# Kernel optimization log

Measured on AMD Instinct MI355X. Metric: run time of the kernel, lower is better.

Reference implementation:

```python
import jax, jax.numpy as jnp
import numpy as np


def setup_inputs() -> dict:
    key = jax.random.key(0)
    ks = jax.random.split(key, 9)
    B, L, D, H, E = 8, 2048, 1024, 256, 8
    Hg = D // 4
    s = 0.02
    return {
        "x": jax.random.normal(ks[0], (B, L, D), dtype=jnp.float32),
        "wg1": jax.random.normal(ks[1], (D, Hg), dtype=jnp.float32) * s,
        "bg1": jax.random.normal(ks[2], (Hg,), dtype=jnp.float32) * s,
        "wg2": jax.random.normal(ks[3], (Hg, E), dtype=jnp.float32) * s,
        "bg2": jax.random.normal(ks[4], (E,), dtype=jnp.float32) * s,
        "w1": jax.random.normal(ks[5], (E, D, H), dtype=jnp.float32) * (1.0 / np.sqrt(D)),
        "b1": jax.random.normal(ks[6], (E, H), dtype=jnp.float32) * s,
        "w2": jax.random.normal(ks[7], (E, H, D), dtype=jnp.float32) * (1.0 / np.sqrt(H)),
        "b2": jax.random.normal(ks[8], (E, D), dtype=jnp.float32) * s,
        "k": 2,
    }


def reference(x, wg1, bg1, wg2, bg2, w1, b1, w2, b2, k):
    B, L, D = x.shape
    xt = x.reshape(-1, D)                       # [T, D] tokens
    T = xt.shape[0]
    # gating MLP: Linear -> GELU(exact, matches torch nn.GELU) -> Linear -> softmax
    logits = jax.nn.gelu(xt @ wg1 + bg1, approximate=False) @ wg2 + bg2  # [T, E]
    scores = jax.nn.softmax(logits, axis=-1)
    top_v, top_i = jax.lax.top_k(scores, k)     # [T, k]
    # dense gate matrix (equivalent to compute_gating's scatter); zeros for non-top-k
    gates = jnp.zeros_like(scores).at[jnp.arange(T)[:, None], top_i].set(top_v)  # [T, E]

    # grouped-GEMM MoE: y[t] = sum_e gates[t,e] * (gelu(x[t] @ W1_e + b1_e) @ W2_e + b2_e)
    # scan over the fixed, small expert axis; gates zero out non-selected experts,
    # giving math identical to the sort/dispatch + per-expert torch.mm loop.
    def body(acc, we):
        w1e, b1e, w2e, b2e, ge = we
        h = jax.nn.gelu(xt @ w1e + b1e, approximate=False)  # [T, H]
        o = h @ w2e + b2e                                    # [T, D]
        return acc + ge[:, None] * o, None

    y, _ = jax.lax.scan(body, jnp.zeros_like(xt), (w1, b1, w2, b2, gates.T))
    return y.reshape(B, L, D)
```

## Files before the change

kernel.cpp:

```cpp
#include <hip/hip_runtime.h>

typedef unsigned short u16;
typedef __attribute__((ext_vector_type(8))) short bf16x8;
typedef __attribute__((ext_vector_type(4))) float f32x4;
typedef __attribute__((ext_vector_type(4))) u16 u16x4;

#define T_TOK 16384
#define D_DIM 1024
#define NE 8
#define MAXP 33792

__device__ __forceinline__ u16 f2bf(float f) {
  union { float f; unsigned int u; } c; c.f = f;
  unsigned int u = c.u;
  u += 0x7fffu + ((u >> 16) & 1u);
  return (u16)(u >> 16);
}

__device__ __forceinline__ float bf2f(u16 v) {
  union { unsigned int u; float f; } c; c.u = ((unsigned int)v) << 16;
  return c.f;
}

__device__ __forceinline__ float gelu_exact(float u) {
  return 0.5f * u * (1.0f + erff(u * 0.70710678118654752f));
}

__device__ __forceinline__ void gld16(const void* g, void* l) {
  __builtin_amdgcn_global_load_lds(
      (const __attribute__((address_space(1))) unsigned int*)g,
      (__attribute__((address_space(3))) unsigned int*)l, 16, 0, 0);
}


__device__ __forceinline__ void stage_tile_swz(u16* lds, const char* g0, size_t stride,
                                               int wid, int lane) {
  const int rg = lane >> 3;
  const int cs = ((lane & 7) ^ rg) * 16;
  const char* g = g0 + (size_t)(wid * 8 + rg) * stride + cs;
  char* l = (char*)lds + wid * 1024;
  #pragma unroll
  for (int c = 0; c < 4; ++c)
    gld16(g + (size_t)(32 * c) * stride, l + c * 4096);
}

__device__ __forceinline__ bf16x8 rd_swz(const u16* lds, int row, int colu16) {
  const int byte = (row * 128 + colu16 * 2) ^ ((row & 7) << 4);
  return *(const bf16x8*)((const char*)lds + byte);
}

__device__ __forceinline__ void mma_step_swz(const u16* As, const u16* Bs, f32x4 acc[4][4],
                                             int wm, int wn, int lane) {
  const int r = lane & 15, kq = (lane >> 4) * 8;
  #pragma unroll
  for (int ks = 0; ks < 2; ++ks) {
    const int col = ks * 32 + kq;
    bf16x8 a[4], b[4];
    #pragma unroll
    for (int mf = 0; mf < 4; ++mf)
      a[mf] = rd_swz(As, wm * 64 + mf * 16 + r, col);
    #pragma unroll
    for (int nf = 0; nf < 4; ++nf)
      b[nf] = rd_swz(Bs, wn * 64 + nf * 16 + r, col);
    #pragma unroll
    for (int mf = 0; mf < 4; ++mf)
      #pragma unroll
      for (int nf = 0; nf < 4; ++nf)
        acc[mf][nf] = __builtin_amdgcn_mfma_f32_16x16x32_bf16(a[mf], b[nf], acc[mf][nf], 0, 0, 0);
  }
}

__device__ __forceinline__ void mma_64x128_swz(const u16* As, const u16* Bs, f32x4 acc[2][4],
                                               int wm, int wn, int lane) {
  const int r = lane & 15, kq = (lane >> 4) * 8;
  #pragma unroll
  for (int ks = 0; ks < 2; ++ks) {
    const int col = ks * 32 + kq;
    bf16x8 a[2], b[4];
    #pragma unroll
    for (int mf = 0; mf < 2; ++mf)
      a[mf] = rd_swz(As, wm * 32 + mf * 16 + r, col);
    #pragma unroll
    for (int nf = 0; nf < 4; ++nf)
      b[nf] = rd_swz(Bs, wn * 64 + nf * 16 + r, col);
    #pragma unroll
    for (int mf = 0; mf < 2; ++mf)
      #pragma unroll
      for (int nf = 0; nf < 4; ++nf)
        acc[mf][nf] = __builtin_amdgcn_mfma_f32_16x16x32_bf16(a[mf], b[nf], acc[mf][nf], 0, 0, 0);
  }
}

__device__ __forceinline__ void stage_b64x32(u16* lds, const u16* mat, int rowbase,
                                             int k0, int wid, int lane) {
  const int row = wid * 16 + (lane >> 2);
  const char* g = (const char*)(mat + (size_t)(rowbase + row) * 1024 + k0 + (lane & 3) * 8);
  char* l = (char*)lds + wid * 1024;
  gld16(g, l);
}

__device__ __forceinline__ void stage_b32(u16* lds, const u16* mat, int rowbase,
                                          int k0, int wid, int lane) {
  const char* g0 = (const char*)(mat + (size_t)rowbase * 1024 + k0);
  #pragma unroll
  for (int c = 0; c < 2; ++c) {
    const int row = c * 64 + wid * 16 + (lane >> 2);
    const char* g = g0 + (size_t)row * 2048 + (size_t)((lane & 3) * 16);
    char* l = (char*)lds + c * 4096 + wid * 1024;
    gld16(g, l);
  }
}

__global__ __launch_bounds__(256) void cvt_hilo_x_kernel(const float* __restrict__ x,
                                                         u16* __restrict__ xh,
                                                         u16* __restrict__ xl) {
  const int i = (blockIdx.x * 256 + threadIdx.x) * 4;
  float4 v = *(const float4*)(x + i);
  float vv[4] = {v.x, v.y, v.z, v.w};
  u16x4 h, l;
  u16 hh[4], ll[4];
  #pragma unroll
  for (int q = 0; q < 4; ++q) { hh[q] = f2bf(vv[q]); ll[q] = f2bf(vv[q] - bf2f(hh[q])); }
  h.x = hh[0]; h.y = hh[1]; h.z = hh[2]; h.w = hh[3];
  l.x = ll[0]; l.y = ll[1]; l.z = ll[2]; l.w = ll[3];
  *(u16x4*)(xh + i) = h;
  *(u16x4*)(xl + i) = l;
}

__global__ __launch_bounds__(256) void transpose_cvt_kernel(const float* __restrict__ in,
                                                            u16* __restrict__ out,
                                                            int R, int C) {
  __shared__ u16 t[32][36];
  const int e = blockIdx.z;
  const int r0 = blockIdx.x * 32, c0 = blockIdx.y * 32;
  const int tid = threadIdx.x;
  {
    const int r = tid >> 3, cq = (tid & 7) * 4;
    float4 v = *(const float4*)(in + ((size_t)e * R + r0 + r) * C + c0 + cq);
    t[r][cq + 0] = f2bf(v.x); t[r][cq + 1] = f2bf(v.y);
    t[r][cq + 2] = f2bf(v.z); t[r][cq + 3] = f2bf(v.w);
  }
  __syncthreads();
  {
    const int c = tid >> 3, rq = (tid & 7) * 4;
    u16x4 o;
    o.x = t[rq + 0][c]; o.y = t[rq + 1][c]; o.z = t[rq + 2][c]; o.w = t[rq + 3][c];
    *(u16x4*)(out + ((size_t)e * C + c0 + c) * R + r0 + rq) = o;
  }
}

__global__ __launch_bounds__(256) void transpose_hilo_kernel(const float* __restrict__ in,
                                                             u16* __restrict__ out_hi,
                                                             u16* __restrict__ out_lo,
                                                             int R, int C) {
  __shared__ u16 th[32][36];
  __shared__ u16 tl[32][36];
  const int r0 = blockIdx.x * 32, c0 = blockIdx.y * 32;
  const int tid = threadIdx.x;
  {
    const int r = tid >> 3, cq = (tid & 7) * 4;
    float4 v = *(const float4*)(in + (size_t)(r0 + r) * C + c0 + cq);
    float vv[4] = {v.x, v.y, v.z, v.w};
    #pragma unroll
    for (int i = 0; i < 4; ++i) {
      u16 h = f2bf(vv[i]);
      th[r][cq + i] = h;
      tl[r][cq + i] = f2bf(vv[i] - bf2f(h));
    }
  }
  __syncthreads();
  {
    const int c = tid >> 3, rq = (tid & 7) * 4;
    u16x4 oh, ol;
    oh.x = th[rq + 0][c]; oh.y = th[rq + 1][c]; oh.z = th[rq + 2][c]; oh.w = th[rq + 3][c];
    ol.x = tl[rq + 0][c]; ol.y = tl[rq + 1][c]; ol.z = tl[rq + 2][c]; ol.w = tl[rq + 3][c];
    *(u16x4*)(out_hi + (size_t)(c0 + c) * R + r0 + rq) = oh;
    *(u16x4*)(out_lo + (size_t)(c0 + c) * R + r0 + rq) = ol;
  }
}

__global__ __launch_bounds__(256) void gating_mfma_kernel(
    const u16* __restrict__ xh, const u16* __restrict__ xl,
    const u16* __restrict__ wg1t_hi, const u16* __restrict__ wg1t_lo,
    float* __restrict__ p_buf) {
  __shared__ u16 Ah[64 * 32], Al[64 * 32];
  __shared__ u16 Bh[128 * 32], Bl[128 * 32];
  const int tid = threadIdx.x, lane = tid & 63, wid = tid >> 6;
  const int t0 = blockIdx.x * 64, n0 = blockIdx.y * 128;
  const int kh = blockIdx.z, kbeg = kh * 512;
  const int wm = wid >> 1, wn = wid & 1;

  f32x4 acc[2][4];
  #pragma unroll
  for (int i = 0; i < 2; ++i)
    #pragma unroll
    for (int j = 0; j < 4; ++j) acc[i][j] = (f32x4){0.f, 0.f, 0.f, 0.f};

  for (int kt = 0; kt < 16; ++kt) {
    const int k0 = kbeg + kt * 32;
    __syncthreads();
    stage_b64x32(Ah, xh, t0, k0, wid, lane);
    stage_b64x32(Al, xl, t0, k0, wid, lane);
    stage_b32(Bh, wg1t_hi, n0, k0, wid, lane);
    stage_b32(Bl, wg1t_lo, n0, k0, wid, lane);
    __syncthreads();
    const int r = lane & 15, ko = (lane >> 4) * 8;
    bf16x8 ah[2], al[2];
    #pragma unroll
    for (int mf = 0; mf < 2; ++mf) {
      const int ro = (wm * 32 + mf * 16 + r) * 32 + ko;
      ah[mf] = *(const bf16x8*)&Ah[ro];
      al[mf] = *(const bf16x8*)&Al[ro];
    }
    #pragma unroll
    for (int nf = 0; nf < 4; ++nf) {
      const int ro = (wn * 64 + nf * 16 + r) * 32 + ko;
      bf16x8 bh = *(const bf16x8*)&Bh[ro];
      bf16x8 bl = *(const bf16x8*)&Bl[ro];
      #pragma unroll
      for (int mf = 0; mf < 2; ++mf) {
        acc[mf][nf] = __builtin_amdgcn_mfma_f32_16x16x32_bf16(ah[mf], bh, acc[mf][nf], 0, 0, 0);
        acc[mf][nf] = __builtin_amdgcn_mfma_f32_16x16x32_bf16(ah[mf], bl, acc[mf][nf], 0, 0, 0);
        acc[mf][nf] = __builtin_amdgcn_mfma_f32_16x16x32_bf16(al[mf], bh, acc[mf][nf], 0, 0, 0);
      }
    }
  }

  #pragma unroll
  for (int mf = 0; mf < 2; ++mf)
    #pragma unroll
    for (int rr = 0; rr < 4; ++rr) {
      const int lt = wm * 32 + mf * 16 + ((lane >> 4) << 2) + rr;
      #pragma unroll
      for (int nf = 0; nf < 4; ++nf) {
        const int ln = wn * 64 + nf * 16 + (lane & 15);
        p_buf[((size_t)kh * T_TOK + t0 + lt) * 256 + n0 + ln] = acc[mf][nf][rr];
      }
    }
}

__global__ __launch_bounds__(256) void gating_p2_kernel(
    const float* __restrict__ p_buf, const float* __restrict__ bg1,
    const float* __restrict__ wg2, const float* __restrict__ bg2,
    int* __restrict__ top_i, float2* __restrict__ top_g) {
  const int tid = threadIdx.x;
  const int tn = tid & 31, tm = tid >> 5;
  const int t0 = blockIdx.x * 32;

  float bb[8];
  {
    float4 ba = *(const float4*)&bg1[tn * 4];
    float4 bc = *(const float4*)&bg1[128 + tn * 4];
    bb[0] = ba.x; bb[1] = ba.y; bb[2] = ba.z; bb[3] = ba.w;
    bb[4] = bc.x; bb[5] = bc.y; bb[6] = bc.z; bb[7] = bc.w;
  }

  float hv[4][8];
  #pragma unroll
  for (int i = 0; i < 4; ++i) {
    const size_t t = t0 + tm * 4 + i;
    const float* pa = &p_buf[t * 256];
    const float* pb = &p_buf[((size_t)T_TOK + t) * 256];
    float4 a0 = *(const float4*)&pa[tn * 4];
    float4 a1 = *(const float4*)&pa[128 + tn * 4];
    float4 b0 = *(const float4*)&pb[tn * 4];
    float4 b1 = *(const float4*)&pb[128 + tn * 4];
    hv[i][0] = gelu_exact(a0.x + b0.x + bb[0]);
    hv[i][1] = gelu_exact(a0.y + b0.y + bb[1]);
    hv[i][2] = gelu_exact(a0.z + b0.z + bb[2]);
    hv[i][3] = gelu_exact(a0.w + b0.w + bb[3]);
    hv[i][4] = gelu_exact(a1.x + b1.x + bb[4]);
    hv[i][5] = gelu_exact(a1.y + b1.y + bb[5]);
    hv[i][6] = gelu_exact(a1.z + b1.z + bb[6]);
    hv[i][7] = gelu_exact(a1.w + b1.w + bb[7]);
  }

  float part[4][8];
  #pragma unroll
  for (int i = 0; i < 4; ++i)
    #pragma unroll
    for (int e = 0; e < 8; ++e) part[i][e] = 0.f;
  #pragma unroll
  for (int j = 0; j < 8; ++j) {
    const int col = (j < 4) ? (tn * 4 + j) : (128 + tn * 4 + (j - 4));
    float4 wa = *(const float4*)&wg2[col * 8];
    float4 wb = *(const float4*)&wg2[col * 8 + 4];
    float we[8] = {wa.x, wa.y, wa.z, wa.w, wb.x, wb.y, wb.z, wb.w};
    #pragma unroll
    for (int i = 0; i < 4; ++i)
      #pragma unroll
      for (int e = 0; e < 8; ++e) part[i][e] += hv[i][j] * we[e];
  }
  #pragma unroll
  for (int mask = 1; mask < 32; mask <<= 1)
    #pragma unroll
    for (int i = 0; i < 4; ++i)
      #pragma unroll
      for (int e = 0; e < 8; ++e) part[i][e] += __shfl_xor(part[i][e], mask);

  if (tn < 4) {
    float lg[8];
    #pragma unroll
    for (int i = 0; i < 4; ++i)
      if (tn == i) {
        #pragma unroll
        for (int e = 0; e < 8; ++e) lg[e] = part[i][e];
      }
    #pragma unroll
    for (int e = 0; e < 8; ++e) lg[e] += bg2[e];
    float m = lg[0];
    #pragma unroll
    for (int e = 1; e < 8; ++e) m = fmaxf(m, lg[e]);
    float ex[8], s = 0.f;
    #pragma unroll
    for (int e = 0; e < 8; ++e) { ex[e] = expf(lg[e] - m); s += ex[e]; }
    int i1 = 0;
    #pragma unroll
    for (int e = 1; e < 8; ++e) if (lg[e] > lg[i1]) i1 = e;
    int i2 = (i1 == 0) ? 1 : 0;
    #pragma unroll
    for (int e = 0; e < 8; ++e) if (e != i1 && lg[e] > lg[i2]) i2 = e;
    float inv = 1.f / s;
    const int t = t0 + tm * 4 + tn;
    top_i[t] = i1 | (i2 << 8);
    top_g[t] = make_float2(ex[i1] * inv, ex[i2] * inv);
  }
}

__global__ __launch_bounds__(256) void hist_kernel(const int* __restrict__ top_i,
                                                   int* __restrict__ hist) {
  __shared__ int h[NE];
  const int tid = threadIdx.x;
  if (tid < NE) h[tid] = 0;
  __syncthreads();
  const int ti = top_i[blockIdx.x * 256 + tid];
  atomicAdd(&h[ti & 255], 1);
  atomicAdd(&h[ti >> 8], 1);
  __syncthreads();
  if (tid < NE) hist[blockIdx.x * NE + tid] = h[tid];
}

__global__ __launch_bounds__(64) void scan_kernel(const int* __restrict__ hist,
                                                  int* __restrict__ cnt,
                                                  int* __restrict__ offs,
                                                  int* __restrict__ cbase) {
  __shared__ int tot[NE], off_s[NE];
  const int tid = threadIdx.x;
  if (tid < NE) {
    int s = 0;
    for (int c = 0; c < 64; ++c) s += hist[c * NE + tid];
    tot[tid] = s; cnt[tid] = s;
  }
  __syncthreads();
  if (tid == 0) {
    int o = 0;
    #pragma unroll
    for (int e = 0; e < NE; ++e) { off_s[e] = o; o += (tot[e] + 127) & ~127; }
  }
  __syncthreads();
  if (tid < NE) {
    offs[tid] = off_s[tid];
    int r = off_s[tid];
    for (int c = 0; c < 64; ++c) { cbase[c * NE + tid] = r; r += hist[c * NE + tid]; }
  }
}

__global__ __launch_bounds__(256) void fill_kernel(
    const int* __restrict__ top_i, const int* __restrict__ cbase,
    int* __restrict__ tok_list, int* __restrict__ pos1, int* __restrict__ pos2) {
  __shared__ int lcnt[NE];
  const int tid = threadIdx.x;
  if (tid < NE) lcnt[tid] = 0;
  __syncthreads();
  const int t = blockIdx.x * 256 + tid;
  const int ti = top_i[t];
  const int i1 = ti & 255, i2 = ti >> 8;
  const int r1 = atomicAdd(&lcnt[i1], 1);
  const int r2 = atomicAdd(&lcnt[i2], 1);
  const int p1 = cbase[blockIdx.x * NE + i1] + r1;
  const int p2 = cbase[blockIdx.x * NE + i2] + r2;
  tok_list[p1] = t; tok_list[p2] = t;
  pos1[t] = p1; pos2[t] = p2;
}

__global__ __launch_bounds__(256) void expert_h_kernel(
    const u16* __restrict__ xb, const u16* __restrict__ w1t,
    const float* __restrict__ b1, const int* __restrict__ tok_list,
    const int* __restrict__ cnt, const int* __restrict__ offs,
    u16* __restrict__ h_c) {
  __shared__ u16 As[64 * 64];
  __shared__ u16 Bs[128 * 64];
  __shared__ float b1_s[128];
  const int e = blockIdx.z;
  const int nblk = (cnt[e] + 63) >> 6;
  if ((int)blockIdx.x >= nblk) return;
  const int tid = threadIdx.x, lane = tid & 63, wid = tid >> 6;
  const int base = offs[e] + blockIdx.x * 64;
  const int n0 = blockIdx.y * 128;
  const int wm = wid >> 1, wn = wid & 1;

  if (tid < 128) b1_s[tid] = b1[e * 256 + n0 + tid];

  int tk[2];
  #pragma unroll
  for (int c = 0; c < 2; ++c)
    tk[c] = tok_list[base + (wid * 2 + c) * 8 + (lane >> 3)];

  f32x4 acc[2][4];
  #pragma unroll
  for (int i = 0; i < 2; ++i)
    #pragma unroll
    for (int j = 0; j < 4; ++j) acc[i][j] = (f32x4){0.f, 0.f, 0.f, 0.f};

  const char* Bb = (const char*)w1t + ((size_t)e * 256 + n0) * 2048;
  const int cb = ((lane & 7) ^ ((lane >> 3) & 7)) * 16;
  for (int kt = 0; kt < 16; ++kt) {
    __syncthreads();
    {
      char* l = (char*)As + wid * 2048;
      #pragma unroll
      for (int c = 0; c < 2; ++c)
        gld16((const char*)xb + (size_t)tk[c] * 2048 + kt * 128 + cb, l + c * 1024);
    }
    stage_tile_swz(Bs, Bb + kt * 128, 2048, wid, lane);
    __syncthreads();
    mma_64x128_swz(As, Bs, acc, wm, wn, lane);
  }

  #pragma unroll
  for (int mf = 0; mf < 2; ++mf)
    #pragma unroll
    for (int rr = 0; rr < 4; ++rr) {
      const int lt = wm * 32 + mf * 16 + ((lane >> 4) << 2) + rr;
      #pragma unroll
      for (int nf = 0; nf < 4; ++nf) {
        const int ln = wn * 64 + nf * 16 + (lane & 15);
        float u = acc[mf][nf][rr] + b1_s[ln];
        h_c[(size_t)(base + lt) * 256 + n0 + ln] = f2bf(gelu_exact(u));
      }
    }
}

__global__ __launch_bounds__(256) void moe_out_kernel(
    const u16* __restrict__ h_c, const u16* __restrict__ w2t,
    const float* __restrict__ b2, const int* __restrict__ cnt,
    const int* __restrict__ offs, u16* __restrict__ o_c) {
  __shared__ u16 As[128 * 64];
  __shared__ u16 Bs[128 * 64];
  __shared__ float b2_s[128];
  const int e = blockIdx.z;
  const int nblk = (cnt[e] + 127) >> 7;
  if ((int)blockIdx.x >= nblk) return;
  const int tid = threadIdx.x, lane = tid & 63, wid = tid >> 6;
  const int base = offs[e] + blockIdx.x * 128;
  const int n0 = blockIdx.y * 128;
  const int wm = wid >> 1, wn = wid & 1;

  if (tid < 128) b2_s[tid] = b2[(size_t)e * 1024 + n0 + tid];

  f32x4 acc[4][4];
  #pragma unroll
  for (int i = 0; i < 4; ++i)
    #pragma unroll
    for (int j = 0; j < 4; ++j) acc[i][j] = (f32x4){0.f, 0.f, 0.f, 0.f};

  const char* Ab = (const char*)h_c + (size_t)base * 512;
  const char* Bb = (const char*)w2t + ((size_t)e * D_DIM + n0) * 512;
  #pragma unroll 1
  for (int kt = 0; kt < 4; ++kt) {
    __syncthreads();
    stage_tile_swz(As, Ab + kt * 128, 512, wid, lane);
    stage_tile_swz(Bs, Bb + kt * 128, 512, wid, lane);
    __syncthreads();
    mma_step_swz(As, Bs, acc, wm, wn, lane);
  }

  #pragma unroll
  for (int mf = 0; mf < 4; ++mf)
    #pragma unroll
    for (int rr = 0; rr < 4; ++rr) {
      const int lt = wm * 64 + mf * 16 + ((lane >> 4) << 2) + rr;
      #pragma unroll
      for (int nf = 0; nf < 4; ++nf) {
        const int ln = wn * 64 + nf * 16 + (lane & 15);
        o_c[(size_t)(base + lt) * 1024 + n0 + ln] = f2bf(acc[mf][nf][rr] + b2_s[ln]);
      }
    }
}

__global__ __launch_bounds__(256) void gather_kernel(
    const u16* __restrict__ o_c, const int* __restrict__ pos1,
    const int* __restrict__ pos2, const float2* __restrict__ top_g,
    float* __restrict__ y) {
  const int t = blockIdx.x;
  const int p1 = pos1[t], p2 = pos2[t];
  const float2 g = top_g[t];
  const int c = threadIdx.x * 4;
  u16x4 a = *(const u16x4*)&o_c[(size_t)p1 * 1024 + c];
  u16x4 b = *(const u16x4*)&o_c[(size_t)p2 * 1024 + c];
  float4 o;
  o.x = g.x * bf2f(a.x) + g.y * bf2f(b.x);
  o.y = g.x * bf2f(a.y) + g.y * bf2f(b.y);
  o.z = g.x * bf2f(a.z) + g.y * bf2f(b.z);
  o.w = g.x * bf2f(a.w) + g.y * bf2f(b.w);
  *(float4*)&y[(size_t)t * 1024 + c] = o;
}

extern "C" void kernel_launch(void* const* d_in, const int* in_sizes, int n_in,
                              void* d_out, int out_size, void* d_ws, size_t ws_size,
                              hipStream_t stream) {
  (void)in_sizes; (void)n_in; (void)out_size; (void)ws_size;
  const float* x   = (const float*)d_in[0];
  const float* wg1 = (const float*)d_in[1];
  const float* bg1 = (const float*)d_in[2];
  const float* wg2 = (const float*)d_in[3];
  const float* bg2 = (const float*)d_in[4];
  const float* w1  = (const float*)d_in[5];
  const float* b1  = (const float*)d_in[6];
  const float* w2  = (const float*)d_in[7];
  const float* b2  = (const float*)d_in[8];
  float* y = (float*)d_out;

  char* ws = (char*)d_ws;
  u16* xb   = (u16*)(ws);
  u16* w1t  = (u16*)(ws + 33554432);
  u16* w2t  = (u16*)(ws + 37748736);
  char* M   = ws + 41943040;
  int*    cnt      = (int*)(M);
  int*    offs     = (int*)(M + 64);
  int*    hist     = (int*)(M + 128);
  int*    cbase    = (int*)(M + 2304);
  int*    tok_list = (int*)(M + 4608);
  int*    top_i    = (int*)(M + 139776);
  float2* top_g    = (float2*)(M + 205312);
  int*    pos1     = (int*)(M + 336384);
  int*    pos2     = (int*)(M + 401920);
  u16* h_c = (u16*)(ws + 42467328);
  u16* o_c = (u16*)(ws + 59768832);
  float* p_buf   = (float*)(ws + 59768832);
  u16*   wg1t_hi = (u16*)(ws + 93323264);
  u16*   wg1t_lo = (u16*)(ws + 93847552);
  u16*   xl      = (u16*)(ws + 94371840);

  hipMemsetAsync(tok_list, 0, 135168, stream);
  cvt_hilo_x_kernel<<<16384, 256, 0, stream>>>(x, xb, xl);
  transpose_cvt_kernel<<<dim3(32, 8, 8), 256, 0, stream>>>(w1, w1t, 1024, 256);
  transpose_cvt_kernel<<<dim3(8, 32, 8), 256, 0, stream>>>(w2, w2t, 256, 1024);
  transpose_hilo_kernel<<<dim3(32, 8), 256, 0, stream>>>(wg1, wg1t_hi, wg1t_lo, 1024, 256);
  gating_mfma_kernel<<<dim3(256, 2, 2), 256, 0, stream>>>(xb, xl, wg1t_hi, wg1t_lo, p_buf);
  gating_p2_kernel<<<512, 256, 0, stream>>>(p_buf, bg1, wg2, bg2, top_i, top_g);
  hist_kernel<<<64, 256, 0, stream>>>(top_i, hist);
  scan_kernel<<<1, 64, 0, stream>>>(hist, cnt, offs, cbase);
  fill_kernel<<<64, 256, 0, stream>>>(top_i, cbase, tok_list, pos1, pos2);
  expert_h_kernel<<<dim3(256, 2, 8), 256, 0, stream>>>(xb, w1t, b1, tok_list, cnt, offs, h_c);
  moe_out_kernel <<<dim3(128, 8, 8), 256, 0, stream>>>(h_c, w2t, b2, cnt, offs, o_c);
  gather_kernel  <<<16384, 256, 0, stream>>>(o_c, pos1, pos2, top_g, y);
}
```

Measured before the change: 195.1 us.

## Fuse expert up-projection and down-projection into one kernel with hidden in LDS

```diff
diff --git a/kernel.cpp b/kernel.cpp
--- a/kernel.cpp
+++ b/kernel.cpp
@@ -49,46 +49,13 @@
   return *(const bf16x8*)((const char*)lds + byte);
 }
 
-__device__ __forceinline__ void mma_step_swz(const u16* As, const u16* Bs, f32x4 acc[4][4],
-                                             int wm, int wn, int lane) {
-  const int r = lane & 15, kq = (lane >> 4) * 8;
-  #pragma unroll
-  for (int ks = 0; ks < 2; ++ks) {
-    const int col = ks * 32 + kq;
-    bf16x8 a[4], b[4];
-    #pragma unroll
-    for (int mf = 0; mf < 4; ++mf)
-      a[mf] = rd_swz(As, wm * 64 + mf * 16 + r, col);
-    #pragma unroll
-    for (int nf = 0; nf < 4; ++nf)
-      b[nf] = rd_swz(Bs, wn * 64 + nf * 16 + r, col);
-    #pragma unroll
-    for (int mf = 0; mf < 4; ++mf)
-      #pragma unroll
-      for (int nf = 0; nf < 4; ++nf)
-        acc[mf][nf] = __builtin_amdgcn_mfma_f32_16x16x32_bf16(a[mf], b[nf], acc[mf][nf], 0, 0, 0);
-  }
-}
-
-__device__ __forceinline__ void mma_64x128_swz(const u16* As, const u16* Bs, f32x4 acc[2][4],
-                                               int wm, int wn, int lane) {
-  const int r = lane & 15, kq = (lane >> 4) * 8;
-  #pragma unroll
-  for (int ks = 0; ks < 2; ++ks) {
-    const int col = ks * 32 + kq;
-    bf16x8 a[2], b[4];
-    #pragma unroll
-    for (int mf = 0; mf < 2; ++mf)
-      a[mf] = rd_swz(As, wm * 32 + mf * 16 + r, col);
-    #pragma unroll
-    for (int nf = 0; nf < 4; ++nf)
-      b[nf] = rd_swz(Bs, wn * 64 + nf * 16 + r, col);
-    #pragma unroll
-    for (int mf = 0; mf < 2; ++mf)
-      #pragma unroll
-      for (int nf = 0; nf < 4; ++nf)
-        acc[mf][nf] = __builtin_amdgcn_mfma_f32_16x16x32_bf16(a[mf], b[nf], acc[mf][nf], 0, 0, 0);
-  }
+__device__ __forceinline__ bf16x8 rd_swz512(const u16* lds, int row, int colu16) {
+  const int byte = (row * 512 + colu16 * 2) ^ ((row & 7) << 4);
+  return *(const bf16x8*)((const char*)lds + byte);
+}
+__device__ __forceinline__ void wr_swz512(u16* lds, int row, int colu16, u16 v) {
+  const int byte = (row * 512 + colu16 * 2) ^ ((row & 7) << 4);
+  *(u16*)((char*)lds + byte) = v;
 }
 
 __device__ __forceinline__ void stage_b64x32(u16* lds, const u16* mat, int rowbase,
@@ -109,6 +76,13 @@
     char* l = (char*)lds + c * 4096 + wid * 1024;
     gld16(g, l);
   }
+}
+
+__device__ __forceinline__ int find_expert(const int* offs, int p0) {
+  int e = 0;
+  #pragma unroll
+  for (int q = 1; q < NE; ++q) if (p0 >= offs[q]) e = q;
+  return e;
 }
 
 __global__ __launch_bounds__(256) void cvt_hilo_x_kernel(const float* __restrict__ x,
@@ -383,109 +357,128 @@
   pos1[t] = p1; pos2[t] = p2;
 }
 
-__global__ __launch_bounds__(256) void expert_h_kernel(
+__global__ __launch_bounds__(256) void fused_expert_kernel(
     const u16* __restrict__ xb, const u16* __restrict__ w1t,
-    const float* __restrict__ b1, const int* __restrict__ tok_list,
+    const u16* __restrict__ w2t, const float* __restrict__ b1,
+    const float* __restrict__ b2, const int* __restrict__ tok_list,
     const int* __restrict__ cnt, const int* __restrict__ offs,
-    u16* __restrict__ h_c) {
-  __shared__ u16 As[64 * 64];
-  __shared__ u16 Bs[128 * 64];
-  __shared__ float b1_s[128];
-  const int e = blockIdx.z;
-  const int nblk = (cnt[e] + 63) >> 6;
-  if ((int)blockIdx.x >= nblk) return;
+    u16* __restrict__ o_c) {
+  __shared__ u16 AB[20480];
+  __shared__ u16 h_lds[64 * 256];
+  __shared__ float b1_s[256];
+  u16* As = AB;
+  u16* Bs = AB + 4096;
+  u16* B2s = AB;
+
   const int tid = threadIdx.x, lane = tid & 63, wid = tid >> 6;
-  const int base = offs[e] + blockIdx.x * 64;
-  const int n0 = blockIdx.y * 128;
+  const int base = blockIdx.x * 64;
+  const int e = find_expert(offs, base);
+  if (base >= offs[e] + ((cnt[e] + 127) & ~127)) return;
   const int wm = wid >> 1, wn = wid & 1;
-
-  if (tid < 128) b1_s[tid] = b1[e * 256 + n0 + tid];
+  const int r = lane & 15, kq = (lane >> 4) * 8;
+
+  b1_s[tid] = b1[e * 256 + tid];
 
   int tk[2];
   #pragma unroll
   for (int c = 0; c < 2; ++c)
     tk[c] = tok_list[base + (wid * 2 + c) * 8 + (lane >> 3)];
-
-  f32x4 acc[2][4];
-  #pragma unroll
-  for (int i = 0; i < 2; ++i)
-    #pragma unroll
-    for (int j = 0; j < 4; ++j) acc[i][j] = (f32x4){0.f, 0.f, 0.f, 0.f};
-
-  const char* Bb = (const char*)w1t + ((size_t)e * 256 + n0) * 2048;
   const int cb = ((lane & 7) ^ ((lane >> 3) & 7)) * 16;
-  for (int kt = 0; kt < 16; ++kt) {
-    __syncthreads();
-    {
-      char* l = (char*)As + wid * 2048;
-      #pragma unroll
-      for (int c = 0; c < 2; ++c)
-        gld16((const char*)xb + (size_t)tk[c] * 2048 + kt * 128 + cb, l + c * 1024);
-    }
-    stage_tile_swz(Bs, Bb + kt * 128, 2048, wid, lane);
-    __syncthreads();
-    mma_64x128_swz(As, Bs, acc, wm, wn, lane);
-  }
-
-  #pragma unroll
-  for (int mf = 0; mf < 2; ++mf)
-    #pragma unroll
-    for (int rr = 0; rr < 4; ++rr) {
-      const int lt = wm * 32 + mf * 16 + ((lane >> 4) << 2) + rr;
-      #pragma unroll
-      for (int nf = 0; nf < 4; ++nf) {
-        const int ln = wn * 64 + nf * 16 + (lane & 15);
-        float u = acc[mf][nf][rr] + b1_s[ln];
-        h_c[(size_t)(base + lt) * 256 + n0 + ln] = f2bf(gelu_exact(u));
-      }
-    }
-}
-
-__global__ __launch_bounds__(256) void moe_out_kernel(
-    const u16* __restrict__ h_c, const u16* __restrict__ w2t,
-    const float* __restrict__ b2, const int* __restrict__ cnt,
-    const int* __restrict__ offs, u16* __restrict__ o_c) {
-  __shared__ u16 As[128 * 64];
-  __shared__ u16 Bs[128 * 64];
-  __shared__ float b2_s[128];
-  const int e = blockIdx.z;
-  const int nblk = (cnt[e] + 127) >> 7;
-  if ((int)blockIdx.x >= nblk) return;
-  const int tid = threadIdx.x, lane = tid & 63, wid = tid >> 6;
-  const int base = offs[e] + blockIdx.x * 128;
-  const int n0 = blockIdx.y * 128;
-  const int wm = wid >> 1, wn = wid & 1;
-
-  if (tid < 128) b2_s[tid] = b2[(size_t)e * 1024 + n0 + tid];
-
-  f32x4 acc[4][4];
-  #pragma unroll
-  for (int i = 0; i < 4; ++i)
-    #pragma unroll
-    for (int j = 0; j < 4; ++j) acc[i][j] = (f32x4){0.f, 0.f, 0.f, 0.f};
-
-  const char* Ab = (const char*)h_c + (size_t)base * 512;
-  const char* Bb = (const char*)w2t + ((size_t)e * D_DIM + n0) * 512;
-  #pragma unroll 1
-  for (int kt = 0; kt < 4; ++kt) {
-    __syncthreads();
-    stage_tile_swz(As, Ab + kt * 128, 512, wid, lane);
-    stage_tile_swz(Bs, Bb + kt * 128, 512, wid, lane);
-    __syncthreads();
-    mma_step_swz(As, Bs, acc, wm, wn, lane);
-  }
-
-  #pragma unroll
-  for (int mf = 0; mf < 4; ++mf)
-    #pragma unroll
-    for (int rr = 0; rr < 4; ++rr) {
-      const int lt = wm * 64 + mf * 16 + ((lane >> 4) << 2) + rr;
-      #pragma unroll
-      for (int nf = 0; nf < 4; ++nf) {
-        const int ln = wn * 64 + nf * 16 + (lane & 15);
-        o_c[(size_t)(base + lt) * 1024 + n0 + ln] = f2bf(acc[mf][nf][rr] + b2_s[ln]);
-      }
-    }
+
+  {
+    f32x4 acc1[2][8];
+    #pragma unroll
+    for (int i = 0; i < 2; ++i)
+      #pragma unroll
+      for (int j = 0; j < 8; ++j) acc1[i][j] = (f32x4){0.f, 0.f, 0.f, 0.f};
+
+    const char* Bb = (const char*)w1t + (size_t)e * 256 * 2048;
+    for (int kt = 0; kt < 16; ++kt) {
+      __syncthreads();
+      {
+        char* l = (char*)As + wid * 2048;
+        #pragma unroll
+        for (int c = 0; c < 2; ++c)
+          gld16((const char*)xb + (size_t)tk[c] * 2048 + kt * 128 + cb, l + c * 1024);
+      }
+      stage_tile_swz(Bs, Bb + kt * 128, 2048, wid, lane);
+      stage_tile_swz(Bs + 128 * 64, Bb + 128 * 2048 + kt * 128, 2048, wid, lane);
+      __syncthreads();
+      #pragma unroll
+      for (int ks = 0; ks < 2; ++ks) {
+        const int col = ks * 32 + kq;
+        bf16x8 a[2], b[8];
+        #pragma unroll
+        for (int mf = 0; mf < 2; ++mf)
+          a[mf] = rd_swz(As, wm * 32 + mf * 16 + r, col);
+        #pragma unroll
+        for (int nf = 0; nf < 8; ++nf)
+          b[nf] = rd_swz(Bs, wn * 128 + nf * 16 + r, col);
+        #pragma unroll
+        for (int mf = 0; mf < 2; ++mf)
+          #pragma unroll
+          for (int nf = 0; nf < 8; ++nf)
+            acc1[mf][nf] = __builtin_amdgcn_mfma_f32_16x16x32_bf16(a[mf], b[nf], acc1[mf][nf], 0, 0, 0);
+      }
+    }
+    #pragma unroll
+    for (int mf = 0; mf < 2; ++mf)
+      #pragma unroll
+      for (int rr = 0; rr < 4; ++rr) {
+        const int row = wm * 32 + mf * 16 + ((lane >> 4) << 2) + rr;
+        #pragma unroll
+        for (int nf = 0; nf < 8; ++nf) {
+          const int colc = wn * 128 + nf * 16 + (lane & 15);
+          float u = acc1[mf][nf][rr] + b1_s[colc];
+          wr_swz512(h_lds, row, colc, f2bf(gelu_exact(u)));
+        }
+      }
+  }
+
+  const char* Wb = (const char*)w2t + (size_t)e * D_DIM * 512;
+  for (int nt = 0; nt < 8; ++nt) {
+    const int n0 = nt * 128;
+    f32x4 acc2[2][4];
+    #pragma unroll
+    for (int i = 0; i < 2; ++i)
+      #pragma unroll
+      for (int j = 0; j < 4; ++j) acc2[i][j] = (f32x4){0.f, 0.f, 0.f, 0.f};
+
+    #pragma unroll 1
+    for (int kt = 0; kt < 4; ++kt) {
+      __syncthreads();
+      stage_tile_swz(B2s, Wb + (size_t)n0 * 512 + kt * 128, 512, wid, lane);
+      __syncthreads();
+      #pragma unroll
+      for (int ks = 0; ks < 2; ++ks) {
+        const int col = ks * 32 + kq;
+        bf16x8 a[2], b[4];
+        #pragma unroll
+        for (int mf = 0; mf < 2; ++mf)
+          a[mf] = rd_swz512(h_lds, wm * 32 + mf * 16 + r, kt * 64 + col);
+        #pragma unroll
+        for (int nf = 0; nf < 4; ++nf)
+          b[nf] = rd_swz(B2s, wn * 64 + nf * 16 + r, col);
+        #pragma unroll
+        for (int mf = 0; mf < 2; ++mf)
+          #pragma unroll
+          for (int nf = 0; nf < 4; ++nf)
+            acc2[mf][nf] = __builtin_amdgcn_mfma_f32_16x16x32_bf16(a[mf], b[nf], acc2[mf][nf], 0, 0, 0);
+      }
+    }
+    #pragma unroll
+    for (int nf = 0; nf < 4; ++nf) {
+      const int ln = wn * 64 + nf * 16 + (lane & 15);
+      const float bv = b2[(size_t)e * 1024 + n0 + ln];
+      #pragma unroll
+      for (int mf = 0; mf < 2; ++mf)
+        #pragma unroll
+        for (int rr = 0; rr < 4; ++rr) {
+          const int lt = wm * 32 + mf * 16 + ((lane >> 4) << 2) + rr;
+          o_c[(size_t)(base + lt) * 1024 + n0 + ln] = f2bf(acc2[mf][nf][rr] + bv);
+        }
+    }
+  }
 }
 
 __global__ __launch_bounds__(256) void gather_kernel(
@@ -535,7 +528,6 @@
   float2* top_g    = (float2*)(M + 205312);
   int*    pos1     = (int*)(M + 336384);
   int*    pos2     = (int*)(M + 401920);
-  u16* h_c = (u16*)(ws + 42467328);
   u16* o_c = (u16*)(ws + 59768832);
   float* p_buf   = (float*)(ws + 59768832);
   u16*   wg1t_hi = (u16*)(ws + 93323264);
@@ -552,7 +544,6 @@
   hist_kernel<<<64, 256, 0, stream>>>(top_i, hist);
   scan_kernel<<<1, 64, 0, stream>>>(hist, cnt, offs, cbase);
   fill_kernel<<<64, 256, 0, stream>>>(top_i, cbase, tok_list, pos1, pos2);
-  expert_h_kernel<<<dim3(256, 2, 8), 256, 0, stream>>>(xb, w1t, b1, tok_list, cnt, offs, h_c);
-  moe_out_kernel <<<dim3(128, 8, 8), 256, 0, stream>>>(h_c, w2t, b2, cnt, offs, o_c);
-  gather_kernel  <<<16384, 256, 0, stream>>>(o_c, pos1, pos2, top_g, y);
-}
+  fused_expert_kernel<<<528, 256, 0, stream>>>(xb, w1t, w2t, b1, b2, tok_list, cnt, offs, o_c);
+  gather_kernel<<<16384, 256, 0, stream>>>(o_c, pos1, pos2, top_g, y);
+}
```

Result: slower. 237.2 us (+21.5%).

## Flatten moe_out grid over padded rows and widen tiles to 128x256 with 8 waves

Applied to the files above, without the earlier changes.

```diff
diff --git a/kernel.cpp b/kernel.cpp
--- a/kernel.cpp
+++ b/kernel.cpp
@@ -44,6 +44,27 @@
     gld16(g + (size_t)(32 * c) * stride, l + c * 4096);
 }
 
+__device__ __forceinline__ void stage_a128_8w(u16* lds, const char* g0, size_t stride,
+                                              int wid, int lane) {
+  const int rg = lane >> 3;
+  const int cs = ((lane & 7) ^ rg) * 16;
+  const char* g = g0 + (size_t)(wid * 16 + rg) * stride + cs;
+  char* l = (char*)lds + wid * 2048;
+  gld16(g, l);
+  gld16(g + (size_t)8 * stride, l + 1024);
+}
+
+__device__ __forceinline__ void stage_b256_8w(u16* lds, const char* g0, size_t stride,
+                                              int wid, int lane) {
+  const int rg = lane >> 3;
+  const int cs = ((lane & 7) ^ rg) * 16;
+  const char* g = g0 + (size_t)(wid * 32 + rg) * stride + cs;
+  char* l = (char*)lds + wid * 4096;
+  #pragma unroll
+  for (int c = 0; c < 4; ++c)
+    gld16(g + (size_t)(8 * c) * stride, l + c * 1024);
+}
+
 __device__ __forceinline__ bf16x8 rd_swz(const u16* lds, int row, int colu16) {
   const int byte = (row * 128 + colu16 * 2) ^ ((row & 7) << 4);
   return *(const bf16x8*)((const char*)lds + byte);
@@ -109,6 +130,13 @@
     char* l = (char*)lds + c * 4096 + wid * 1024;
     gld16(g, l);
   }
+}
+
+__device__ __forceinline__ int find_expert(const int* offs, int p0) {
+  int e = 0;
+  #pragma unroll
+  for (int q = 1; q < NE; ++q) if (p0 >= offs[q]) e = q;
+  return e;
 }
 
 __global__ __launch_bounds__(256) void cvt_hilo_x_kernel(const float* __restrict__ x,
@@ -441,22 +469,19 @@
     }
 }
 
-__global__ __launch_bounds__(256) void moe_out_kernel(
+__global__ __launch_bounds__(512) void moe_out_kernel(
     const u16* __restrict__ h_c, const u16* __restrict__ w2t,
     const float* __restrict__ b2, const int* __restrict__ cnt,
     const int* __restrict__ offs, u16* __restrict__ o_c) {
   __shared__ u16 As[128 * 64];
-  __shared__ u16 Bs[128 * 64];
-  __shared__ float b2_s[128];
-  const int e = blockIdx.z;
-  const int nblk = (cnt[e] + 127) >> 7;
-  if ((int)blockIdx.x >= nblk) return;
+  __shared__ u16 Bs[256 * 64];
   const int tid = threadIdx.x, lane = tid & 63, wid = tid >> 6;
-  const int base = offs[e] + blockIdx.x * 128;
-  const int n0 = blockIdx.y * 128;
-  const int wm = wid >> 1, wn = wid & 1;
-
-  if (tid < 128) b2_s[tid] = b2[(size_t)e * 1024 + n0 + tid];
+  const int base = blockIdx.x * 128;
+  const int e = find_expert(offs, base);
+  if (base >= offs[e] + ((cnt[e] + 127) & ~127)) return;
+  const int n0 = blockIdx.y * 256;
+  const int wm = wid >> 2, wn = wid & 3;
+  const int r = lane & 15, kq = (lane >> 4) * 8;
 
   f32x4 acc[4][4];
   #pragma unroll
@@ -469,23 +494,39 @@
   #pragma unroll 1
   for (int kt = 0; kt < 4; ++kt) {
     __syncthreads();
-    stage_tile_swz(As, Ab + kt * 128, 512, wid, lane);
-    stage_tile_swz(Bs, Bb + kt * 128, 512, wid, lane);
+    stage_a128_8w(As, Ab + kt * 128, 512, wid, lane);
+    stage_b256_8w(Bs, Bb + kt * 128, 512, wid, lane);
     __syncthreads();
-    mma_step_swz(As, Bs, acc, wm, wn, lane);
-  }
-
-  #pragma unroll
-  for (int mf = 0; mf < 4; ++mf)
-    #pragma unroll
-    for (int rr = 0; rr < 4; ++rr) {
-      const int lt = wm * 64 + mf * 16 + ((lane >> 4) << 2) + rr;
-      #pragma unroll
-      for (int nf = 0; nf < 4; ++nf) {
-        const int ln = wn * 64 + nf * 16 + (lane & 15);
-        o_c[(size_t)(base + lt) * 1024 + n0 + ln] = f2bf(acc[mf][nf][rr] + b2_s[ln]);
+    #pragma unroll
+    for (int ks = 0; ks < 2; ++ks) {
+      const int col = ks * 32 + kq;
+      bf16x8 a[4], b[4];
+      #pragma unroll
+      for (int mf = 0; mf < 4; ++mf)
+        a[mf] = rd_swz(As, wm * 64 + mf * 16 + r, col);
+      #pragma unroll
+      for (int nf = 0; nf < 4; ++nf)
+        b[nf] = rd_swz(Bs, wn * 64 + nf * 16 + r, col);
+      #pragma unroll
+      for (int mf = 0; mf < 4; ++mf)
+        #pragma unroll
+        for (int nf = 0; nf < 4; ++nf)
+          acc[mf][nf] = __builtin_amdgcn_mfma_f32_16x16x32_bf16(a[mf], b[nf], acc[mf][nf], 0, 0, 0);
+    }
+  }
+
+  #pragma unroll
+  for (int nf = 0; nf < 4; ++nf) {
+    const int ln = wn * 64 + nf * 16 + (lane & 15);
+    const float bv = b2[(size_t)e * 1024 + n0 + ln];
+    #pragma unroll
+    for (int mf = 0; mf < 4; ++mf)
+      #pragma unroll
+      for (int rr = 0; rr < 4; ++rr) {
+        const int lt = wm * 64 + mf * 16 + ((lane >> 4) << 2) + rr;
+        o_c[(size_t)(base + lt) * 1024 + n0 + ln] = f2bf(acc[mf][nf][rr] + bv);
       }
-    }
+  }
 }
 
 __global__ __launch_bounds__(256) void gather_kernel(
@@ -553,6 +594,6 @@
   scan_kernel<<<1, 64, 0, stream>>>(hist, cnt, offs, cbase);
   fill_kernel<<<64, 256, 0, stream>>>(top_i, cbase, tok_list, pos1, pos2);
   expert_h_kernel<<<dim3(256, 2, 8), 256, 0, stream>>>(xb, w1t, b1, tok_list, cnt, offs, h_c);
-  moe_out_kernel <<<dim3(128, 8, 8), 256, 0, stream>>>(h_c, w2t, b2, cnt, offs, o_c);
-  gather_kernel  <<<16384, 256, 0, stream>>>(o_c, pos1, pos2, top_g, y);
-}
+  moe_out_kernel<<<dim3(264, 4), 512, 0, stream>>>(h_c, w2t, b2, cnt, offs, o_c);
+  gather_kernel<<<16384, 256, 0, stream>>>(o_c, pos1, pos2, top_g, y);
+}
```

Result: no change. 191.5 us (-1.9%).
